# Kernel optimization log

Hardware: AMD Instinct MI355X
Metric: run time of the kernel (lower is better)

Reference implementation:

```python
import jax, jax.numpy as jnp
import numpy as np

DIM = 256
D_STATE = 64
D_CONV = 4
EXPAND = 2
D_INNER = EXPAND * DIM          # 512
DT_RANK = DIM // 16             # 16, Mamba default dt_rank='auto'
LN_EPS = 1e-5


def setup_inputs() -> dict:
    key = jax.random.key(0)
    ks = jax.random.split(key, 8)
    B, L = 4, 1024
    s = lambda k, shape, fan: jax.random.normal(k, shape, jnp.float32) / np.sqrt(fan).astype(np.float32)
    inp = {}
    inp['x'] = jax.random.normal(ks[0], (B, L, DIM), jnp.float32)
    inp['C_SA'] = jax.random.normal(ks[1], (B, L, D_STATE), jnp.float32)
    # LayerNorm params
    inp['gamma'] = jnp.ones((DIM,), jnp.float32)
    inp['beta'] = jnp.zeros((DIM,), jnp.float32)
    # Mamba params
    inp['W_in'] = s(ks[2], (2 * D_INNER, DIM), DIM)
    inp['conv_w'] = s(ks[3], (D_INNER, 1, D_CONV), D_CONV)   # depthwise causal conv
    inp['conv_b'] = jnp.zeros((D_INNER,), jnp.float32)
    inp['W_x'] = s(ks[4], (DT_RANK + D_STATE, D_INNER), D_INNER)  # -> (dt_low_rank, B_ssm)
    inp['W_dt'] = s(ks[5], (D_INNER, DT_RANK), DT_RANK)
    # softplus-inverse of 0.01 so initial dt ~ 0.01 (Mamba dt init)
    inp['b_dt'] = jnp.log(jnp.expm1(jnp.full((D_INNER,), 0.01, jnp.float32)))
    # S4D-real init: A = -[1..N]
    inp['A_log'] = jnp.log(jnp.broadcast_to(jnp.arange(1, D_STATE + 1, dtype=jnp.float32), (D_INNER, D_STATE)))
    inp['D'] = jnp.ones((D_INNER,), jnp.float32)
    inp['W_out'] = s(ks[6], (DIM, D_INNER), D_INNER)
    return inp


def reference(x, C_SA, gamma, beta, W_in, conv_w, conv_b, W_x, W_dt, b_dt, A_log, D, W_out):
    B, L, _ = x.shape
    # --- LayerNorm ---
    mu = jnp.mean(x, axis=-1, keepdims=True)
    var = jnp.mean(jnp.square(x - mu), axis=-1, keepdims=True)
    xn = (x - mu) * jax.lax.rsqrt(var + LN_EPS) * gamma + beta
    # --- input projection and gate split ---
    xz = xn @ W_in.T                              # [B,L,2*Di]
    u, z = jnp.split(xz, 2, axis=-1)
    # --- causal depthwise conv1d + SiLU ---
    u_c = jax.lax.conv_general_dilated(
        u.transpose(0, 2, 1), conv_w, (1,), [(D_CONV - 1, 0)],
        feature_group_count=D_INNER,
        dimension_numbers=('NCH', 'OIH', 'NCH'))  # [B,Di,L]
    u = jax.nn.silu(u_c.transpose(0, 2, 1) + conv_b)  # [B,L,Di]
    # --- data-dependent SSM params (C comes from C_SA externally) ---
    dbl = u @ W_x.T                               # [B,L,dt_rank+N]
    dt = jax.nn.softplus(dbl[..., :DT_RANK] @ W_dt.T + b_dt)  # [B,L,Di]
    Bs = dbl[..., DT_RANK:]                       # [B,L,N]
    A = -jnp.exp(A_log)                           # [Di,N]
    # --- selective scan over time ---
    def step(h, t):
        dt_t, B_t, C_t, u_t = t                   # [B,Di],[B,N],[B,N],[B,Di]
        dA = jnp.exp(dt_t[..., None] * A)         # [B,Di,N]
        h = dA * h + (dt_t * u_t)[..., None] * B_t[:, None, :]
        y = jnp.einsum('bdn,bn->bd', h, C_t)
        return h, y
    h0 = jnp.zeros((B, D_INNER, D_STATE), x.dtype)
    xs = (dt.transpose(1, 0, 2), Bs.transpose(1, 0, 2),
          C_SA.transpose(1, 0, 2), u.transpose(1, 0, 2))
    _, ys = jax.lax.scan(step, h0, xs)            # ys: [L,B,Di]
    y = ys.transpose(1, 0, 2) + u * D             # skip connection
    y = y * jax.nn.silu(z)                        # gate
    return y @ W_out.T                            # [B,L,dim]
```

## Files before the change

### kernel.cpp

```cpp
#include <hip/hip_runtime.h>
#include <cstdint>
#include <cstddef>

#define B_    4
#define L_    1024
#define DIM_  256
#define DI_   512
#define NTOK  (B_*L_)
#define NC    32
#define CL    (L_/NC)

__device__ __forceinline__ float siluf_(float x){ return x / (1.0f + __expf(-x)); }
__device__ __forceinline__ float softplusf_(float x){
  return (x > 15.0f) ? x : log1pf(__expf(x));
}

__global__ __launch_bounds__(1024) void k_check(const float* __restrict__ A_log,
    int* __restrict__ flag){
  __shared__ int s_ok;
  int tid = threadIdx.x;
  if (tid == 0) s_ok = 1;
  __syncthreads();
  int ok = 1;
  for (int i = tid; i < 512 * 64; i += 1024){
    int n = i & 63;
    float ref = logf((float)(n + 1));
    float v = A_log[i];
    if (fabsf(v - ref) > 1e-5f * fmaxf(1.0f, fabsf(ref))) ok = 0;
  }
  if (!ok) atomicAnd(&s_ok, 0);
  __syncthreads();
  if (tid == 0) *flag = s_ok;
}

__global__ __launch_bounds__(256) void k_ln_stats(const float* __restrict__ x,
    float* __restrict__ stats){
  int tok  = blockIdx.x * 4 + (threadIdx.x >> 6);
  int lane = threadIdx.x & 63;
  float4 v = *(const float4*)(x + (size_t)tok * DIM_ + lane * 4);
  float s  = v.x + v.y + v.z + v.w;
  float sq = v.x*v.x + v.y*v.y + v.z*v.z + v.w*v.w;
  #pragma unroll
  for (int off = 32; off; off >>= 1){
    s  += __shfl_xor(s,  off, 64);
    sq += __shfl_xor(sq, off, 64);
  }
  if (lane == 0){
    float mu = s * (1.0f / DIM_);
    stats[tok*2]   = mu;
    stats[tok*2+1] = rsqrtf(sq * (1.0f / DIM_) - mu*mu + 1e-5f);
  }
}

__global__ __launch_bounds__(256) void k_gemm1(const float* __restrict__ x,
    const float* __restrict__ stats, const float* __restrict__ gamma,
    const float* __restrict__ beta, const float* __restrict__ Win,
    float* __restrict__ xz){
  __shared__ float As[16 * 68];
  __shared__ float Bs[16 * 68];
  int tid = threadIdx.x;
  int mBase = blockIdx.y * 64;
  int nBase = blockIdx.x * 64;
  int tx = tid & 15, ty = tid >> 4;
  int am = tid >> 2, ak = (tid & 3) << 2;
  float mu = stats[(mBase+am)*2], rs = stats[(mBase+am)*2+1];
  float acc[4][4] = {};
  const float* xp = x   + (size_t)(mBase+am)*256 + ak;
  const float* wp = Win + (size_t)(nBase+am)*256 + ak;
  float4 av = *(const float4*)(xp);
  float4 bv = *(const float4*)(wp);
  float4 gv = *(const float4*)(gamma + ak);
  float4 be = *(const float4*)(beta  + ak);
  for (int kt = 0; kt < 256; kt += 16){
    As[(ak+0)*68+am] = (av.x - mu) * rs * gv.x + be.x;
    As[(ak+1)*68+am] = (av.y - mu) * rs * gv.y + be.y;
    As[(ak+2)*68+am] = (av.z - mu) * rs * gv.z + be.z;
    As[(ak+3)*68+am] = (av.w - mu) * rs * gv.w + be.w;
    Bs[(ak+0)*68+am]=bv.x; Bs[(ak+1)*68+am]=bv.y;
    Bs[(ak+2)*68+am]=bv.z; Bs[(ak+3)*68+am]=bv.w;
    __syncthreads();
    float4 avN, bvN, gvN, beN;
    if (kt + 16 < 256){
      avN = *(const float4*)(xp + kt + 16);
      bvN = *(const float4*)(wp + kt + 16);
      gvN = *(const float4*)(gamma + kt + 16 + ak);
      beN = *(const float4*)(beta  + kt + 16 + ak);
    }
    #pragma unroll
    for (int kk = 0; kk < 16; kk++){
      float4 a = *(const float4*)&As[kk*68 + ty*4];
      float4 b = *(const float4*)&Bs[kk*68 + tx*4];
      float ar[4] = {a.x,a.y,a.z,a.w}, br[4] = {b.x,b.y,b.z,b.w};
      #pragma unroll
      for (int i=0;i<4;i++)
        #pragma unroll
        for (int j=0;j<4;j++)
          acc[i][j] += ar[i]*br[j];
    }
    __syncthreads();
    av = avN; bv = bvN; gv = gvN; be = beN;
  }
  #pragma unroll
  for (int i=0;i<4;i++){
    float4 o = make_float4(acc[i][0],acc[i][1],acc[i][2],acc[i][3]);
    *(float4*)(xz + (size_t)(mBase+ty*4+i)*1024 + nBase + tx*4) = o;
  }
}

__global__ __launch_bounds__(256) void k_conv(const float* __restrict__ xz,
    const float* __restrict__ cw, const float* __restrict__ cb,
    float* __restrict__ uc){
  int g = blockIdx.x * 256 + threadIdx.x;
  int d = g & 511;
  int tok = g >> 9;
  int t = tok & (L_ - 1);
  float w0 = cw[d*4+0], w1 = cw[d*4+1], w2 = cw[d*4+2], w3 = cw[d*4+3];
  const float* up = xz + (size_t)tok * 1024 + d;
  float acc = cb[d] + w3 * up[0];
  if (t >= 1) acc += w2 * up[-1 * 1024];
  if (t >= 2) acc += w1 * up[-2 * 1024];
  if (t >= 3) acc += w0 * up[-3 * 1024];
  uc[g] = siluf_(acc);
}

__global__ __launch_bounds__(320) void k_gemm2(const float* __restrict__ uc,
    const float* __restrict__ Wx, float* __restrict__ dbl){
  __shared__ float As[4 * 516];
  int tid = threadIdx.x;
  int mBase = blockIdx.x * 4;
  for (int idx = tid * 4; idx < 4 * 512; idx += 320 * 4){
    int r = idx >> 9, k = idx & 511;
    *(float4*)&As[r * 516 + k] = *(const float4*)(uc + (size_t)(mBase + r) * 512 + k);
  }
  __syncthreads();
  int n = tid >> 2;
  int r = tid & 3;
  const float* arow = &As[r * 516];
  const float* wp = Wx + (size_t)n * 512;
  float acc = 0.f;
  #pragma unroll 8
  for (int k4 = 0; k4 < 512; k4 += 4){
    float4 a = *(const float4*)&arow[k4];
    float4 w = *(const float4*)(wp + k4);
    acc += a.x*w.x + a.y*w.y + a.z*w.z + a.w*w.w;
  }
  dbl[(size_t)(mBase + r) * 80 + n] = acc;
}

__global__ __launch_bounds__(256) void k_dt(const float* __restrict__ dbl,
    const float* __restrict__ Wdt, const float* __restrict__ bdt,
    float* __restrict__ dt){
  int g = blockIdx.x * 256 + threadIdx.x;
  int d = g & 511; int m = g >> 9;
  float acc = bdt[d];
  const float* r = dbl + (size_t)m * 80;
  #pragma unroll
  for (int k = 0; k < 16; k++)
    acc += r[k] * Wdt[d * 16 + k];
  dt[g] = softplusf_(acc);
}

__global__ __launch_bounds__(256, 4) void k_scanA(const float* __restrict__ dt,
    const float* __restrict__ uc, const float* __restrict__ dbl,
    const float* __restrict__ A_log, const int* __restrict__ flagp,
    float* __restrict__ hseg, float* __restrict__ S){
  __shared__ float sB[CL][64];
  __shared__ float sDt[CL][32];
  __shared__ float sU[CL][32];
  int tid  = threadIdx.x;
  int gw   = (blockIdx.x * 256 + tid) >> 6;
  int lane = tid & 63;
  int dsub = lane & 7, ngrp = lane >> 3;
  int grp = gw & 255;
  int c   = gw >> 8;
  int ch  = grp * 8 + dsub;
  int b = ch >> 9, d = ch & 511;
  int tbeg = c * CL;
  int ch0 = ((blockIdx.x * 4) & 255) * 8;
  int d0  = ch0 & 511;
  {
    const float* Bsrc = dbl + (size_t)b * L_ * 80 + (size_t)tbeg * 80 + 16;
    for (int i = tid; i < CL * 16; i += 256){
      int row = i >> 4, col = (i & 15) << 2;
      *(float4*)&sB[row][col] = *(const float4*)(Bsrc + row * 80 + col);
    }
    const float* Dsrc = dt + (size_t)b * L_ * 512 + (size_t)tbeg * 512 + d0;
    const float* Usrc = uc + (size_t)b * L_ * 512 + (size_t)tbeg * 512 + d0;
    int zr = tid >> 3, zc = (tid & 7) << 2;
    *(float4*)&sDt[zr][zc] = *(const float4*)(Dsrc + zr * 512 + zc);
    *(float4*)&sU[zr][zc]  = *(const float4*)(Usrc + zr * 512 + zc);
  }
  __syncthreads();
  int fast = *flagp;
  int lch = (grp & 3) * 8 + dsub;
  float h[8] = {};
  float Ssum = 0.f;
  float st1 = (float)(ngrp * 8 + 1);
  if (fast){
    for (int tt = 0; tt < CL; tt += 4){
      #pragma unroll
      for (int j = 0; j < 4; j++){
        float dtv = sDt[tt+j][lch];
        float uv  = sU[tt+j][lch];
        float4 b0 = *(const float4*)&sB[tt+j][ngrp*8];
        float4 b1 = *(const float4*)&sB[tt+j][ngrp*8+4];
        float sc = dtv * uv;
        Ssum += dtv;
        float e1 = __expf(-dtv);
        float e2 = e1 * e1;
        float e4 = e2 * e2;
        float dA0 = __expf(-dtv * st1);
        float dA1 = dA0 * e1;
        float dA2 = dA0 * e2;
        float dA3 = dA1 * e2;
        h[0] = dA0 * h[0] + sc * b0.x;
        h[1] = dA1 * h[1] + sc * b0.y;
        h[2] = dA2 * h[2] + sc * b0.z;
        h[3] = dA3 * h[3] + sc * b0.w;
        dA0 *= e4; dA1 *= e4; dA2 *= e4; dA3 *= e4;
        h[4] = dA0 * h[4] + sc * b1.x;
        h[5] = dA1 * h[5] + sc * b1.y;
        h[6] = dA2 * h[6] + sc * b1.z;
        h[7] = dA3 * h[7] + sc * b1.w;
      }
    }
  } else {
    float Aa[8];
    float4 a0 = *(const float4*)(A_log + (size_t)d*64 + ngrp*8);
    float4 a1 = *(const float4*)(A_log + (size_t)d*64 + ngrp*8 + 4);
    Aa[0]=-__expf(a0.x); Aa[1]=-__expf(a0.y); Aa[2]=-__expf(a0.z); Aa[3]=-__expf(a0.w);
    Aa[4]=-__expf(a1.x); Aa[5]=-__expf(a1.y); Aa[6]=-__expf(a1.z); Aa[7]=-__expf(a1.w);
    for (int tt = 0; tt < CL; tt += 4){
      #pragma unroll
      for (int j = 0; j < 4; j++){
        float dtv = sDt[tt+j][lch];
        float uv  = sU[tt+j][lch];
        float4 b0 = *(const float4*)&sB[tt+j][ngrp*8];
        float4 b1 = *(const float4*)&sB[tt+j][ngrp*8+4];
        float Bv[8] = {b0.x,b0.y,b0.z,b0.w,b1.x,b1.y,b1.z,b1.w};
        float sc = dtv * uv;
        Ssum += dtv;
        #pragma unroll
        for (int i = 0; i < 8; i++)
          h[i] = __expf(dtv * Aa[i]) * h[i] + sc * Bv[i];
      }
    }
  }
  float* hp = hseg + ((size_t)(c * 2048 + ch)) * 64 + ngrp*8;
  *(float4*)hp     = make_float4(h[0],h[1],h[2],h[3]);
  *(float4*)(hp+4) = make_float4(h[4],h[5],h[6],h[7]);
  if (ngrp == 0) S[c * 2048 + ch] = Ssum;
}

__global__ __launch_bounds__(256) void k_scanB(float* __restrict__ hseg,
    const float* __restrict__ S, const float* __restrict__ A_log,
    const int* __restrict__ flagp){
  int ch   = (blockIdx.x * 256 + threadIdx.x) >> 6;
  int lane = threadIdx.x & 63;
  int d = ch & 511;
  int fast = *flagp;
  float A = fast ? -(float)(lane + 1) : -__expf(A_log[(size_t)d * 64 + lane]);
  float hc = 0.f;
  #pragma unroll 8
  for (int c = 0; c < NC; c++){
    size_t idx = ((size_t)(c * 2048 + ch)) * 64 + lane;
    float hf = hseg[idx];
    hseg[idx] = hc;
    float Sv = S[c * 2048 + ch];
    hc = hf + __expf(A * Sv) * hc;
  }
}

__global__ __launch_bounds__(256, 4) void k_scanC(const float* __restrict__ dt,
    const float* __restrict__ uc, const float* __restrict__ dbl,
    const float* __restrict__ C_SA, const float* __restrict__ A_log,
    const int* __restrict__ flagp,
    const float* __restrict__ hin, const float* __restrict__ xz,
    const float* __restrict__ Dp, float* __restrict__ ys){
  __shared__ float sB[CL][64];
  __shared__ float sC[CL][64];
  __shared__ float sZ[CL][32];
  __shared__ float sDt[CL][32];
  __shared__ float sU[CL][32];
  int tid  = threadIdx.x;
  int gw   = (blockIdx.x * 256 + tid) >> 6;
  int lane = tid & 63;
  int dsub = lane & 7, ngrp = lane >> 3;
  int grp = gw & 255;
  int c   = gw >> 8;
  int ch  = grp * 8 + dsub;
  int b = ch >> 9, d = ch & 511;
  int tbeg = c * CL;
  int ch0 = ((blockIdx.x * 4) & 255) * 8;
  int d0  = ch0 & 511;
  {
    const float* Bsrc = dbl  + (size_t)b * L_ * 80 + (size_t)tbeg * 80 + 16;
    const float* Csrc = C_SA + (size_t)b * L_ * 64 + (size_t)tbeg * 64;
    for (int i = tid; i < CL * 16; i += 256){
      int row = i >> 4, col = (i & 15) << 2;
      *(float4*)&sB[row][col] = *(const float4*)(Bsrc + row * 80 + col);
      *(float4*)&sC[row][col] = *(const float4*)(Csrc + row * 64 + col);
    }
    const float* Zsrc = xz + (size_t)b * L_ * 1024 + (size_t)tbeg * 1024 + 512 + d0;
    const float* Dsrc = dt + (size_t)b * L_ * 512 + (size_t)tbeg * 512 + d0;
    const float* Usrc = uc + (size_t)b * L_ * 512 + (size_t)tbeg * 512 + d0;
    int zr = tid >> 3, zc = (tid & 7) << 2;
    *(float4*)&sZ[zr][zc]  = *(const float4*)(Zsrc + zr * 1024 + zc);
    *(float4*)&sDt[zr][zc] = *(const float4*)(Dsrc + zr * 512 + zc);
    *(float4*)&sU[zr][zc]  = *(const float4*)(Usrc + zr * 512 + zc);
  }
  __syncthreads();
  int fast = *flagp;
  float Dv = Dp[d];
  int lch = (grp & 3) * 8 + dsub;
  float*       yw  = ys + (size_t)b * L_ * 512 + d;
  float h[8];
  {
    const float* hp = hin + ((size_t)(c * 2048 + ch)) * 64 + ngrp*8;
    float4 h0 = *(const float4*)hp;
    float4 h1 = *(const float4*)(hp + 4);
    h[0]=h0.x; h[1]=h0.y; h[2]=h0.z; h[3]=h0.w;
    h[4]=h1.x; h[5]=h1.y; h[6]=h1.z; h[7]=h1.w;
  }
  float st1 = (float)(ngrp * 8 + 1);
  if (fast){
    for (int tt = 0; tt < CL; tt += 4){
      float yp[4], uj[4];
      #pragma unroll
      for (int j = 0; j < 4; j++){
        float dtv = sDt[tt+j][lch];
        float uv  = sU[tt+j][lch];
        uj[j] = uv;
        float4 b0 = *(const float4*)&sB[tt+j][ngrp*8];
        float4 b1 = *(const float4*)&sB[tt+j][ngrp*8+4];
        float4 c0 = *(const float4*)&sC[tt+j][ngrp*8];
        float4 c1 = *(const float4*)&sC[tt+j][ngrp*8+4];
        float sc = dtv * uv;
        float e1 = __expf(-dtv);
        float e2 = e1 * e1;
        float e4 = e2 * e2;
        float dA0 = __expf(-dtv * st1);
        float dA1 = dA0 * e1;
        float dA2 = dA0 * e2;
        float dA3 = dA1 * e2;
        h[0] = dA0 * h[0] + sc * b0.x;
        h[1] = dA1 * h[1] + sc * b0.y;
        h[2] = dA2 * h[2] + sc * b0.z;
        h[3] = dA3 * h[3] + sc * b0.w;
        float y0 = h[0] * c0.x;
        float y1 = h[1] * c0.y;
        float y2 = h[2] * c0.z;
        float y3 = h[3] * c0.w;
        dA0 *= e4; dA1 *= e4; dA2 *= e4; dA3 *= e4;
        h[4] = dA0 * h[4] + sc * b1.x;
        h[5] = dA1 * h[5] + sc * b1.y;
        h[6] = dA2 * h[6] + sc * b1.z;
        h[7] = dA3 * h[7] + sc * b1.w;
        y0 += h[4] * c1.x;
        y1 += h[5] * c1.y;
        y2 += h[6] * c1.z;
        y3 += h[7] * c1.w;
        yp[j] = (y0 + y1) + (y2 + y3);
      }
      #pragma unroll
      for (int off = 8; off < 64; off <<= 1){
        #pragma unroll
        for (int j = 0; j < 4; j++)
          yp[j] += __shfl_xor(yp[j], off, 64);
      }
      if (ngrp == 0){
        #pragma unroll
        for (int j = 0; j < 4; j++){
          float z = sZ[tt+j][lch];
          yw[(size_t)(tbeg+tt+j) * 512] = (yp[j] + uj[j] * Dv) * siluf_(z);
        }
      }
    }
  } else {
    float Aa[8];
    float4 a0 = *(const float4*)(A_log + (size_t)d*64 + ngrp*8);
    float4 a1 = *(const float4*)(A_log + (size_t)d*64 + ngrp*8 + 4);
    Aa[0]=-__expf(a0.x); Aa[1]=-__expf(a0.y); Aa[2]=-__expf(a0.z); Aa[3]=-__expf(a0.w);
    Aa[4]=-__expf(a1.x); Aa[5]=-__expf(a1.y); Aa[6]=-__expf(a1.z); Aa[7]=-__expf(a1.w);
    for (int tt = 0; tt < CL; tt += 4){
      float yp[4], uj[4];
      #pragma unroll
      for (int j = 0; j < 4; j++){
        float dtv = sDt[tt+j][lch];
        float uv  = sU[tt+j][lch];
        uj[j] = uv;
        float4 b0 = *(const float4*)&sB[tt+j][ngrp*8];
        float4 b1 = *(const float4*)&sB[tt+j][ngrp*8+4];
        float4 c0 = *(const float4*)&sC[tt+j][ngrp*8];
        float4 c1 = *(const float4*)&sC[tt+j][ngrp*8+4];
        float sc = dtv * uv;
        h[0] = __expf(dtv * Aa[0]) * h[0] + sc * b0.x;
        h[1] = __expf(dtv * Aa[1]) * h[1] + sc * b0.y;
        h[2] = __expf(dtv * Aa[2]) * h[2] + sc * b0.z;
        h[3] = __expf(dtv * Aa[3]) * h[3] + sc * b0.w;
        float y0 = h[0] * c0.x;
        float y1 = h[1] * c0.y;
        float y2 = h[2] * c0.z;
        float y3 = h[3] * c0.w;
        h[4] = __expf(dtv * Aa[4]) * h[4] + sc * b1.x;
        h[5] = __expf(dtv * Aa[5]) * h[5] + sc * b1.y;
        h[6] = __expf(dtv * Aa[6]) * h[6] + sc * b1.z;
        h[7] = __expf(dtv * Aa[7]) * h[7] + sc * b1.w;
        y0 += h[4] * c1.x;
        y1 += h[5] * c1.y;
        y2 += h[6] * c1.z;
        y3 += h[7] * c1.w;
        yp[j] = (y0 + y1) + (y2 + y3);
      }
      #pragma unroll
      for (int off = 8; off < 64; off <<= 1){
        #pragma unroll
        for (int j = 0; j < 4; j++)
          yp[j] += __shfl_xor(yp[j], off, 64);
      }
      if (ngrp == 0){
        #pragma unroll
        for (int j = 0; j < 4; j++){
          float z = sZ[tt+j][lch];
          yw[(size_t)(tbeg+tt+j) * 512] = (yp[j] + uj[j] * Dv) * siluf_(z);
        }
      }
    }
  }
}

__global__ __launch_bounds__(256) void k_gemm3s(const float* __restrict__ Ag,
    const float* __restrict__ Wout, float* __restrict__ pbuf){
  __shared__ float As[16 * 68];
  __shared__ float Bs[16 * 68];
  int tid = threadIdx.x;
  int nBase = blockIdx.x * 64;
  int mBase = blockIdx.y * 64;
  int kBase = blockIdx.z * 128;
  int tx = tid & 15, ty = tid >> 4;
  int am = tid >> 2, ak = (tid & 3) << 2;
  float acc[4][4] = {};
  const float* ap = Ag   + (size_t)(mBase+am)*512 + ak;
  const float* wp = Wout + (size_t)(nBase+am)*512 + ak;
  float4 av = *(const float4*)(ap + kBase);
  float4 bv = *(const float4*)(wp + kBase);
  for (int kt = kBase; kt < kBase + 128; kt += 16){
    As[(ak+0)*68+am]=av.x; As[(ak+1)*68+am]=av.y;
    As[(ak+2)*68+am]=av.z; As[(ak+3)*68+am]=av.w;
    Bs[(ak+0)*68+am]=bv.x; Bs[(ak+1)*68+am]=bv.y;
    Bs[(ak+2)*68+am]=bv.z; Bs[(ak+3)*68+am]=bv.w;
    __syncthreads();
    float4 avN, bvN;
    if (kt + 16 < kBase + 128){
      avN = *(const float4*)(ap + kt + 16);
      bvN = *(const float4*)(wp + kt + 16);
    }
    #pragma unroll
    for (int kk = 0; kk < 16; kk++){
      float4 a = *(const float4*)&As[kk*68 + ty*4];
      float4 b = *(const float4*)&Bs[kk*68 + tx*4];
      float ar[4] = {a.x,a.y,a.z,a.w}, br[4] = {b.x,b.y,b.z,b.w};
      #pragma unroll
      for (int i=0;i<4;i++)
        #pragma unroll
        for (int j=0;j<4;j++)
          acc[i][j] += ar[i]*br[j];
    }
    __syncthreads();
    av = avN; bv = bvN;
  }
  float* pw = pbuf + (size_t)blockIdx.z * (NTOK * 256);
  #pragma unroll
  for (int i=0;i<4;i++){
    float4 o = make_float4(acc[i][0],acc[i][1],acc[i][2],acc[i][3]);
    *(float4*)(pw + (size_t)(mBase+ty*4+i)*256 + nBase + tx*4) = o;
  }
}

__global__ __launch_bounds__(256) void k_g3red(const float* __restrict__ pbuf,
    float* __restrict__ out){
  int i4 = (blockIdx.x * 256 + threadIdx.x) * 4;
  float4 a = *(const float4*)(pbuf + i4);
  float4 b = *(const float4*)(pbuf + (size_t)NTOK*256   + i4);
  float4 c = *(const float4*)(pbuf + (size_t)NTOK*512   + i4);
  float4 d = *(const float4*)(pbuf + (size_t)NTOK*768   + i4);
  float4 o = make_float4((a.x+b.x)+(c.x+d.x), (a.y+b.y)+(c.y+d.y),
                         (a.z+b.z)+(c.z+d.z), (a.w+b.w)+(c.w+d.w));
  *(float4*)(out + i4) = o;
}

extern "C" void kernel_launch(void* const* d_in, const int* in_sizes, int n_in,
                              void* d_out, int out_size, void* d_ws, size_t ws_size,
                              hipStream_t stream) {
  const float* x      = (const float*)d_in[0];
  const float* C_SA   = (const float*)d_in[1];
  const float* gamma  = (const float*)d_in[2];
  const float* beta   = (const float*)d_in[3];
  const float* W_in   = (const float*)d_in[4];
  const float* conv_w = (const float*)d_in[5];
  const float* conv_b = (const float*)d_in[6];
  const float* W_x    = (const float*)d_in[7];
  const float* W_dt   = (const float*)d_in[8];
  const float* b_dt   = (const float*)d_in[9];
  const float* A_log  = (const float*)d_in[10];
  const float* Dw     = (const float*)d_in[11];
  const float* W_out  = (const float*)d_in[12];
  float* out = (float*)d_out;

  float* ws    = (float*)d_ws;
  float* stats = ws;
  int*   flag  = (int*)(ws + 8192);
  float* xz    = ws    + 16384;
  float* uc    = xz    + 4194304;
  float* dbl   = uc    + 2097152;
  float* dtb   = dbl   + 327680;
  float* hseg  = dtb   + 2097152;
  float* S     = hseg  + 4194304;
  float* ysb   = S     + 65536;
  float* pbuf  = hseg;

  k_check<<<1, 1024, 0, stream>>>(A_log, flag);
  k_ln_stats<<<NTOK/4, 256, 0, stream>>>(x, stats);
  k_gemm1<<<dim3(16, 64), 256, 0, stream>>>(x, stats, gamma, beta, W_in, xz);
  k_conv <<<(NTOK*512)/256, 256, 0, stream>>>(xz, conv_w, conv_b, uc);
  k_gemm2<<<1024, 320, 0, stream>>>(uc, W_x, dbl);
  k_dt   <<<(NTOK*512)/256, 256, 0, stream>>>(dbl, W_dt, b_dt, dtb);
  k_scanA<<<NC*64, 256, 0, stream>>>(dtb, uc, dbl, A_log, flag, hseg, S);
  k_scanB<<<512, 256, 0, stream>>>(hseg, S, A_log, flag);
  k_scanC<<<NC*64, 256, 0, stream>>>(dtb, uc, dbl, C_SA, A_log, flag, hseg, xz, Dw, ysb);
  k_gemm3s<<<dim3(4, 64, 4), 256, 0, stream>>>(ysb, W_out, pbuf);
  k_g3red<<<NTOK*256/1024, 256, 0, stream>>>(pbuf, out);
}
```

Before: 242.8 us.

## Double-buffer shared tiles in GEMMs and fuse dt projection into gemm2

The input and output projection GEMMs now use two shared-memory tile buffers, so the next tile is written while the current one is consumed, leaving one barrier per k-step instead of two. The dt projection and softplus are folded into the x-projection kernel, which keeps the 16 dt-rank values in shared memory and removes a separate launch and a reread of dbl. The x-projection dot product is also split across four independent accumulators to shorten the dependency chain. The cost is extra LDS use for the double buffers and more serial work per block in gemm2.

```diff
diff --git a/kernel.cpp b/kernel.cpp
--- a/kernel.cpp
+++ b/kernel.cpp
@@ -56,8 +56,8 @@
     const float* __restrict__ stats, const float* __restrict__ gamma,
     const float* __restrict__ beta, const float* __restrict__ Win,
     float* __restrict__ xz){
-  __shared__ float As[16 * 68];
-  __shared__ float Bs[16 * 68];
+  __shared__ float As[2][16 * 68];
+  __shared__ float Bs[2][16 * 68];
   int tid = threadIdx.x;
   int mBase = blockIdx.y * 64;
   int nBase = blockIdx.x * 64;
@@ -67,20 +67,24 @@
   float acc[4][4] = {};
   const float* xp = x   + (size_t)(mBase+am)*256 + ak;
   const float* wp = Win + (size_t)(nBase+am)*256 + ak;
-  float4 av = *(const float4*)(xp);
-  float4 bv = *(const float4*)(wp);
-  float4 gv = *(const float4*)(gamma + ak);
-  float4 be = *(const float4*)(beta  + ak);
+  {
+    float4 av = *(const float4*)(xp);
+    float4 bv = *(const float4*)(wp);
+    float4 gv = *(const float4*)(gamma + ak);
+    float4 be = *(const float4*)(beta  + ak);
+    As[0][(ak+0)*68+am] = (av.x - mu) * rs * gv.x + be.x;
+    As[0][(ak+1)*68+am] = (av.y - mu) * rs * gv.y + be.y;
+    As[0][(ak+2)*68+am] = (av.z - mu) * rs * gv.z + be.z;
+    As[0][(ak+3)*68+am] = (av.w - mu) * rs * gv.w + be.w;
+    Bs[0][(ak+0)*68+am]=bv.x; Bs[0][(ak+1)*68+am]=bv.y;
+    Bs[0][(ak+2)*68+am]=bv.z; Bs[0][(ak+3)*68+am]=bv.w;
+  }
+  __syncthreads();
+  int cur = 0;
   for (int kt = 0; kt < 256; kt += 16){
-    As[(ak+0)*68+am] = (av.x - mu) * rs * gv.x + be.x;
-    As[(ak+1)*68+am] = (av.y - mu) * rs * gv.y + be.y;
-    As[(ak+2)*68+am] = (av.z - mu) * rs * gv.z + be.z;
-    As[(ak+3)*68+am] = (av.w - mu) * rs * gv.w + be.w;
-    Bs[(ak+0)*68+am]=bv.x; Bs[(ak+1)*68+am]=bv.y;
-    Bs[(ak+2)*68+am]=bv.z; Bs[(ak+3)*68+am]=bv.w;
-    __syncthreads();
+    bool has = (kt + 16) < 256;
     float4 avN, bvN, gvN, beN;
-    if (kt + 16 < 256){
+    if (has){
       avN = *(const float4*)(xp + kt + 16);
       bvN = *(const float4*)(wp + kt + 16);
       gvN = *(const float4*)(gamma + kt + 16 + ak);
@@ -88,8 +92,8 @@
     }
     #pragma unroll
     for (int kk = 0; kk < 16; kk++){
-      float4 a = *(const float4*)&As[kk*68 + ty*4];
-      float4 b = *(const float4*)&Bs[kk*68 + tx*4];
+      float4 a = *(const float4*)&As[cur][kk*68 + ty*4];
+      float4 b = *(const float4*)&Bs[cur][kk*68 + tx*4];
       float ar[4] = {a.x,a.y,a.z,a.w}, br[4] = {b.x,b.y,b.z,b.w};
       #pragma unroll
       for (int i=0;i<4;i++)
@@ -97,8 +101,17 @@
         for (int j=0;j<4;j++)
           acc[i][j] += ar[i]*br[j];
     }
-    __syncthreads();
-    av = avN; bv = bvN; gv = gvN; be = beN;
+    if (has){
+      int nxt = cur ^ 1;
+      As[nxt][(ak+0)*68+am] = (avN.x - mu) * rs * gvN.x + beN.x;
+      As[nxt][(ak+1)*68+am] = (avN.y - mu) * rs * gvN.y + beN.y;
+      As[nxt][(ak+2)*68+am] = (avN.z - mu) * rs * gvN.z + beN.z;
+      As[nxt][(ak+3)*68+am] = (avN.w - mu) * rs * gvN.w + beN.w;
+      Bs[nxt][(ak+0)*68+am]=bvN.x; Bs[nxt][(ak+1)*68+am]=bvN.y;
+      Bs[nxt][(ak+2)*68+am]=bvN.z; Bs[nxt][(ak+3)*68+am]=bvN.w;
+      __syncthreads();
+      cur = nxt;
+    }
   }
   #pragma unroll
   for (int i=0;i<4;i++){
@@ -124,8 +137,11 @@
 }
 
 __global__ __launch_bounds__(320) void k_gemm2(const float* __restrict__ uc,
-    const float* __restrict__ Wx, float* __restrict__ dbl){
+    const float* __restrict__ Wx, const float* __restrict__ Wdt,
+    const float* __restrict__ bdt, float* __restrict__ dbl,
+    float* __restrict__ dtb){
   __shared__ float As[4 * 516];
+  __shared__ __align__(16) float sD[4][16];
   int tid = threadIdx.x;
   int mBase = blockIdx.x * 4;
   for (int idx = tid * 4; idx < 4 * 512; idx += 320 * 4){
@@ -137,27 +153,39 @@
   int r = tid & 3;
   const float* arow = &As[r * 516];
   const float* wp = Wx + (size_t)n * 512;
-  float acc = 0.f;
-  #pragma unroll 8
-  for (int k4 = 0; k4 < 512; k4 += 4){
-    float4 a = *(const float4*)&arow[k4];
-    float4 w = *(const float4*)(wp + k4);
-    acc += a.x*w.x + a.y*w.y + a.z*w.z + a.w*w.w;
-  }
+  float acc0 = 0.f, acc1 = 0.f, acc2 = 0.f, acc3 = 0.f;
+  #pragma unroll 4
+  for (int k = 0; k < 512; k += 16){
+    float4 a0 = *(const float4*)&arow[k];
+    float4 w0 = *(const float4*)(wp + k);
+    float4 a1 = *(const float4*)&arow[k+4];
+    float4 w1 = *(const float4*)(wp + k+4);
+    float4 a2 = *(const float4*)&arow[k+8];
+    float4 w2 = *(const float4*)(wp + k+8);
+    float4 a3 = *(const float4*)&arow[k+12];
+    float4 w3 = *(const float4*)(wp + k+12);
+    acc0 += a0.x*w0.x + a0.y*w0.y + a0.z*w0.z + a0.w*w0.w;
+    acc1 += a1.x*w1.x + a1.y*w1.y + a1.z*w1.z + a1.w*w1.w;
+    acc2 += a2.x*w2.x + a2.y*w2.y + a2.z*w2.z + a2.w*w2.w;
+    acc3 += a3.x*w3.x + a3.y*w3.y + a3.z*w3.z + a3.w*w3.w;
+  }
+  float acc = (acc0 + acc1) + (acc2 + acc3);
   dbl[(size_t)(mBase + r) * 80 + n] = acc;
-}
-
-__global__ __launch_bounds__(256) void k_dt(const float* __restrict__ dbl,
-    const float* __restrict__ Wdt, const float* __restrict__ bdt,
-    float* __restrict__ dt){
-  int g = blockIdx.x * 256 + threadIdx.x;
-  int d = g & 511; int m = g >> 9;
-  float acc = bdt[d];
-  const float* r = dbl + (size_t)m * 80;
-  #pragma unroll
-  for (int k = 0; k < 16; k++)
-    acc += r[k] * Wdt[d * 16 + k];
-  dt[g] = softplusf_(acc);
+  if (n < 16) sD[r][n] = acc;
+  __syncthreads();
+  for (int i = tid; i < 4 * 512; i += 320){
+    int rr = i >> 9, d = i & 511;
+    const float4* wd = (const float4*)(Wdt + d * 16);
+    const float4* dd = (const float4*)&sD[rr][0];
+    float4 w0 = wd[0], w1 = wd[1], w2 = wd[2], w3 = wd[3];
+    float4 d0 = dd[0], d1 = dd[1], d2 = dd[2], d3 = dd[3];
+    float p0 = d0.x*w0.x + d0.y*w0.y + d0.z*w0.z + d0.w*w0.w;
+    float p1 = d1.x*w1.x + d1.y*w1.y + d1.z*w1.z + d1.w*w1.w;
+    float p2 = d2.x*w2.x + d2.y*w2.y + d2.z*w2.z + d2.w*w2.w;
+    float p3 = d3.x*w3.x + d3.y*w3.y + d3.z*w3.z + d3.w*w3.w;
+    float a = bdt[d] + (p0 + p1) + (p2 + p3);
+    dtb[(size_t)(mBase + rr) * 512 + d] = softplusf_(a);
+  }
 }
 
 __global__ __launch_bounds__(256, 4) void k_scanA(const float* __restrict__ dt,
@@ -431,8 +459,8 @@
 
 __global__ __launch_bounds__(256) void k_gemm3s(const float* __restrict__ Ag,
     const float* __restrict__ Wout, float* __restrict__ pbuf){
-  __shared__ float As[16 * 68];
-  __shared__ float Bs[16 * 68];
+  __shared__ float As[2][16 * 68];
+  __shared__ float Bs[2][16 * 68];
   int tid = threadIdx.x;
   int nBase = blockIdx.x * 64;
   int mBase = blockIdx.y * 64;
@@ -442,23 +470,27 @@
   float acc[4][4] = {};
   const float* ap = Ag   + (size_t)(mBase+am)*512 + ak;
   const float* wp = Wout + (size_t)(nBase+am)*512 + ak;
-  float4 av = *(const float4*)(ap + kBase);
-  float4 bv = *(const float4*)(wp + kBase);
+  {
+    float4 av = *(const float4*)(ap + kBase);
+    float4 bv = *(const float4*)(wp + kBase);
+    As[0][(ak+0)*68+am]=av.x; As[0][(ak+1)*68+am]=av.y;
+    As[0][(ak+2)*68+am]=av.z; As[0][(ak+3)*68+am]=av.w;
+    Bs[0][(ak+0)*68+am]=bv.x; Bs[0][(ak+1)*68+am]=bv.y;
+    Bs[0][(ak+2)*68+am]=bv.z; Bs[0][(ak+3)*68+am]=bv.w;
+  }
+  __syncthreads();
+  int cur = 0;
   for (int kt = kBase; kt < kBase + 128; kt += 16){
-    As[(ak+0)*68+am]=av.x; As[(ak+1)*68+am]=av.y;
-    As[(ak+2)*68+am]=av.z; As[(ak+3)*68+am]=av.w;
-    Bs[(ak+0)*68+am]=bv.x; Bs[(ak+1)*68+am]=bv.y;
-    Bs[(ak+2)*68+am]=bv.z; Bs[(ak+3)*68+am]=bv.w;
-    __syncthreads();
+    bool has = (kt + 16) < kBase + 128;
     float4 avN, bvN;
-    if (kt + 16 < kBase + 128){
+    if (has){
       avN = *(const float4*)(ap + kt + 16);
       bvN = *(const float4*)(wp + kt + 16);
     }
     #pragma unroll
     for (int kk = 0; kk < 16; kk++){
-      float4 a = *(const float4*)&As[kk*68 + ty*4];
-      float4 b = *(const float4*)&Bs[kk*68 + tx*4];
+      float4 a = *(const float4*)&As[cur][kk*68 + ty*4];
+      float4 b = *(const float4*)&Bs[cur][kk*68 + tx*4];
       float ar[4] = {a.x,a.y,a.z,a.w}, br[4] = {b.x,b.y,b.z,b.w};
       #pragma unroll
       for (int i=0;i<4;i++)
@@ -466,8 +498,15 @@
         for (int j=0;j<4;j++)
           acc[i][j] += ar[i]*br[j];
     }
-    __syncthreads();
-    av = avN; bv = bvN;
+    if (has){
+      int nxt = cur ^ 1;
+      As[nxt][(ak+0)*68+am]=avN.x; As[nxt][(ak+1)*68+am]=avN.y;
+      As[nxt][(ak+2)*68+am]=avN.z; As[nxt][(ak+3)*68+am]=avN.w;
+      Bs[nxt][(ak+0)*68+am]=bvN.x; Bs[nxt][(ak+1)*68+am]=bvN.y;
+      Bs[nxt][(ak+2)*68+am]=bvN.z; Bs[nxt][(ak+3)*68+am]=bvN.w;
+      __syncthreads();
+      cur = nxt;
+    }
   }
   float* pw = pbuf + (size_t)blockIdx.z * (NTOK * 256);
   #pragma unroll
@@ -523,8 +562,7 @@
   k_ln_stats<<<NTOK/4, 256, 0, stream>>>(x, stats);
   k_gemm1<<<dim3(16, 64), 256, 0, stream>>>(x, stats, gamma, beta, W_in, xz);
   k_conv <<<(NTOK*512)/256, 256, 0, stream>>>(xz, conv_w, conv_b, uc);
-  k_gemm2<<<1024, 320, 0, stream>>>(uc, W_x, dbl);
-  k_dt   <<<(NTOK*512)/256, 256, 0, stream>>>(dbl, W_dt, b_dt, dtb);
+  k_gemm2<<<1024, 320, 0, stream>>>(uc, W_x, W_dt, b_dt, dbl, dtb);
   k_scanA<<<NC*64, 256, 0, stream>>>(dtb, uc, dbl, A_log, flag, hseg, S);
   k_scanB<<<512, 256, 0, stream>>>(hseg, S, A_log, flag);
   k_scanC<<<NC*64, 256, 0, stream>>>(dtb, uc, dbl, C_SA, A_log, flag, hseg, xz, Dw, ysb);
```

Result: no change. 246.3 us (+1.4%).
